# Kernel tuning notes

Measured on AMD Instinct MI355X. Metric: run time of the kernel, lower is better.

The kernel has to match this reference:

```python
import jax, jax.numpy as jnp
import numpy as np

D = 100  # hard-coded model dim from the source
L, BS = 4096, 64


def setup_inputs() -> dict:
    key = jax.random.key(0)
    k_x, k_w, k_b, k_s = jax.random.split(key, 4)
    x = jax.random.normal(k_x, (L, BS, 1, D), dtype=jnp.float32)
    # nn.Linear(D, D): weight [D, D] (out, in), bias [D]
    lim = 1.0 / np.sqrt(D)
    W = jax.random.uniform(k_w, (D, D), dtype=jnp.float32, minval=-lim, maxval=lim)
    b = jax.random.uniform(k_b, (D,), dtype=jnp.float32, minval=-lim, maxval=lim)
    # self.states ~ Normal(0, 0.02), shape [D, D]
    states = 0.02 * jax.random.normal(k_s, (D, D), dtype=jnp.float32)
    return {"x": x, "W": W, "b": b, "states": states}


def reference(x, W, b, states):
    # z1 = layer1(x): x [L, BS, 1, D] @ W.T + b
    z1 = jnp.einsum("lbod,ed->lboe", x, W) + b
    # scan: carry = tile(states) is constant across steps (f multiplies by 1.0),
    # so output[i] = z1[i] @ states for every timestep -> one fused batched matmul.
    out = jnp.einsum("lbod,de->lboe", z1, states)
    return out
```

## Files before the change

kernel.cpp:

```cpp
#include <hip/hip_runtime.h>

typedef __bf16 bf16x8 __attribute__((ext_vector_type(8)));
typedef float  f32x4  __attribute__((ext_vector_type(4)));

#define D100 100
#define NROWS (4096*64)
#define NTILES (NROWS/16)
#define NCT 7
#define NKS 4
#define FRAG_ELEMS (NCT*NKS*64*8)
#define NBLK (NTILES/8)

__global__ __launch_bounds__(256) void prep_kernel(
    const float* __restrict__ W, const float* __restrict__ bvec,
    const float* __restrict__ S, __bf16* __restrict__ wsM) {
  int tid = blockIdx.x * 256 + threadIdx.x;
  if (tid >= FRAG_ELEMS) return;
  int j    = tid & 7;
  int lane = (tid >> 3) & 63;
  int ks   = (tid >> 9) & 3;
  int ct   = tid >> 11;
  int k = ks * 32 + ((lane >> 4) * 8) + j;
  int n = ct * 16 + (lane & 15);
  float acc = 0.f;
  if (n < D100) {
    if (k < D100) {
      float a0 = 0.f, a1 = 0.f, a2 = 0.f, a3 = 0.f;
      for (int d = 0; d < D100; d += 4) {
        a0 += W[(d + 0) * D100 + k] * S[(d + 0) * D100 + n];
        a1 += W[(d + 1) * D100 + k] * S[(d + 1) * D100 + n];
        a2 += W[(d + 2) * D100 + k] * S[(d + 2) * D100 + n];
        a3 += W[(d + 3) * D100 + k] * S[(d + 3) * D100 + n];
      }
      acc = (a0 + a1) + (a2 + a3);
    } else if (k == 112) {
      for (int d = 0; d < D100; ++d) acc += bvec[d] * S[d * D100 + n];
    }
  }
  wsM[tid] = (__bf16)acc;
}

__global__ __launch_bounds__(512, 8) void gemm_kernel(
    const float* __restrict__ x, const __bf16* __restrict__ wsM,
    float* __restrict__ out) {
  __shared__ __align__(16) __bf16 ldsB[FRAG_ELEMS];

  const int t    = threadIdx.x;
  const int lane = t & 63;
  const int l16  = lane & 15;
  const int lg   = lane >> 4;
  const int tile = blockIdx.x * 8 + (t >> 6);

  const float* xr = x + (size_t)tile * (16 * D100) + l16 * D100;
  f32x4 xv[7];
#pragma unroll
  for (int ks = 0; ks < 3; ++ks) {
    xv[ks * 2]     = *(const f32x4*)(xr + ks * 32 + lg * 8);
    xv[ks * 2 + 1] = *(const f32x4*)(xr + ks * 32 + lg * 8 + 4);
  }
  xv[6] = (lg == 0) ? *(const f32x4*)(xr + 96) : (f32x4){0.f, 0.f, 0.f, 0.f};

  {
    const f32x4* src = (const f32x4*)wsM;
    f32x4*       dst = (f32x4*)ldsB;
    dst[t]        = src[t];
    dst[512 + t]  = src[512 + t];
    dst[1024 + t] = src[1024 + t];
    if (t < 256) dst[1536 + t] = src[1536 + t];
  }
  __syncthreads();

  f32x4 acc[NCT];
#pragma unroll
  for (int ct = 0; ct < NCT; ++ct) acc[ct] = (f32x4){0.f, 0.f, 0.f, 0.f};

  const bf16x8* Bv = (const bf16x8*)ldsB;
#pragma unroll
  for (int ks = 0; ks < NKS; ++ks) {
    bf16x8 xf;
    if (ks < 3) {
      f32x4 v0 = xv[ks * 2], v1 = xv[ks * 2 + 1];
#pragma unroll
      for (int j = 0; j < 4; ++j) {
        xf[j]     = (__bf16)v0[j];
        xf[j + 4] = (__bf16)v1[j];
      }
    } else {
      f32x4 v0 = xv[6];
#pragma unroll
      for (int j = 0; j < 4; ++j) {
        xf[j]     = (__bf16)v0[j];
        xf[j + 4] = (__bf16)0.f;
      }
      if (lg == 2) xf[0] = (__bf16)1.0f;
    }
#pragma unroll
    for (int ct = 0; ct < NCT; ++ct)
      acc[ct] = __builtin_amdgcn_mfma_f32_16x16x32_bf16(
          Bv[(ct * NKS + ks) * 64 + lane], xf, acc[ct], 0, 0, 0);
  }

  float* orow = out + (size_t)tile * (16 * D100) + l16 * D100 + lg * 4;
#pragma unroll
  for (int ct = 0; ct < NCT; ++ct) {
    if (ct < 6 || lg == 0)
      *(f32x4*)(orow + ct * 16) = acc[ct];
  }
}

extern "C" void kernel_launch(void* const* d_in, const int* in_sizes, int n_in,
                              void* d_out, int out_size, void* d_ws,
                              size_t ws_size, hipStream_t stream) {
  const float* x = (const float*)d_in[0];
  const float* W = (const float*)d_in[1];
  const float* b = (const float*)d_in[2];
  const float* S = (const float*)d_in[3];
  __bf16* wsM = (__bf16*)d_ws;
  float*  out = (float*)d_out;

  hipLaunchKernelGGL(prep_kernel, dim3(56), dim3(256), 0, stream,
                     W, b, S, wsM);
  hipLaunchKernelGGL(gemm_kernel, dim3(NBLK), dim3(512), 0, stream,
                     x, wsM, out);
}
```

Baseline: 49.85 us.

## Stage x tiles and output through LDS with direct global-to-LDS loads

Replaces the per-lane strided row loads of x with direct global_load_lds copies of each wave's contiguous 6400-byte tile into shared memory, then reads MFMA operands from LDS. The B fragments are loaded the same way. Results are written to LDS and then stored to global memory as fully contiguous 16-byte-per-lane chunks, so loads and stores are coalesced. This adds 51KB of LDS per block and lowers the occupancy hint from 8 to 4, which may reduce latency hiding.

```diff
diff --git a/kernel.cpp b/kernel.cpp
--- a/kernel.cpp
+++ b/kernel.cpp
@@ -9,7 +9,11 @@
 #define NCT 7
 #define NKS 4
 #define FRAG_ELEMS (NCT*NKS*64*8)
+#define TILE_B 6400
 #define NBLK (NTILES/8)
+
+typedef const __attribute__((address_space(1))) void gvoid;
+typedef __attribute__((address_space(3))) void lvoid;
 
 __global__ __launch_bounds__(256) void prep_kernel(
     const float* __restrict__ W, const float* __restrict__ bvec,
@@ -40,33 +44,35 @@
   wsM[tid] = (__bf16)acc;
 }
 
-__global__ __launch_bounds__(512, 8) void gemm_kernel(
+__global__ __launch_bounds__(512, 4) void gemm_kernel(
     const float* __restrict__ x, const __bf16* __restrict__ wsM,
     float* __restrict__ out) {
   __shared__ __align__(16) __bf16 ldsB[FRAG_ELEMS];
+  __shared__ __align__(16) float  ldsX[8 * 1600];
 
   const int t    = threadIdx.x;
   const int lane = t & 63;
   const int l16  = lane & 15;
   const int lg   = lane >> 4;
-  const int tile = blockIdx.x * 8 + (t >> 6);
+  const int w    = t >> 6;
+  const int tile = blockIdx.x * 8 + w;
 
-  const float* xr = x + (size_t)tile * (16 * D100) + l16 * D100;
-  f32x4 xv[7];
+  const char* xsrc = (const char*)x + (size_t)tile * TILE_B + (size_t)lane * 16;
+  char* ldsx = (char*)(ldsX + w * 1600);
 #pragma unroll
-  for (int ks = 0; ks < 3; ++ks) {
-    xv[ks * 2]     = *(const f32x4*)(xr + ks * 32 + lg * 8);
-    xv[ks * 2 + 1] = *(const f32x4*)(xr + ks * 32 + lg * 8 + 4);
-  }
-  xv[6] = (lg == 0) ? *(const f32x4*)(xr + 96) : (f32x4){0.f, 0.f, 0.f, 0.f};
+  for (int c = 0; c < 6; ++c)
+    __builtin_amdgcn_global_load_lds((gvoid*)(xsrc + c * 1024),
+                                     (lvoid*)(ldsx + c * 1024), 16, 0, 0);
+  if (lane < 16)
+    __builtin_amdgcn_global_load_lds((gvoid*)(xsrc + 6144),
+                                     (lvoid*)(ldsx + 6144), 16, 0, 0);
 
   {
-    const f32x4* src = (const f32x4*)wsM;
-    f32x4*       dst = (f32x4*)ldsB;
-    dst[t]        = src[t];
-    dst[512 + t]  = src[512 + t];
-    dst[1024 + t] = src[1024 + t];
-    if (t < 256) dst[1536 + t] = src[1536 + t];
+    const char* bsrc = (const char*)wsM + (size_t)lane * 16;
+    for (int c = w; c < 28; c += 8)
+      __builtin_amdgcn_global_load_lds((gvoid*)(bsrc + c * 1024),
+                                       (lvoid*)((char*)ldsB + c * 1024),
+                                       16, 0, 0);
   }
   __syncthreads();
 
@@ -75,18 +81,22 @@
   for (int ct = 0; ct < NCT; ++ct) acc[ct] = (f32x4){0.f, 0.f, 0.f, 0.f};
 
   const bf16x8* Bv = (const bf16x8*)ldsB;
+  const char* xrow = ldsx + l16 * 400;
+
 #pragma unroll
   for (int ks = 0; ks < NKS; ++ks) {
     bf16x8 xf;
     if (ks < 3) {
-      f32x4 v0 = xv[ks * 2], v1 = xv[ks * 2 + 1];
+      f32x4 v0 = *(const f32x4*)(xrow + ks * 128 + lg * 32);
+      f32x4 v1 = *(const f32x4*)(xrow + ks * 128 + lg * 32 + 16);
 #pragma unroll
       for (int j = 0; j < 4; ++j) {
         xf[j]     = (__bf16)v0[j];
         xf[j + 4] = (__bf16)v1[j];
       }
     } else {
-      f32x4 v0 = xv[6];
+      f32x4 v0 = (lg == 0) ? *(const f32x4*)(xrow + 384)
+                           : (f32x4){0.f, 0.f, 0.f, 0.f};
 #pragma unroll
       for (int j = 0; j < 4; ++j) {
         xf[j]     = (__bf16)v0[j];
@@ -100,11 +110,21 @@
           Bv[(ct * NKS + ks) * 64 + lane], xf, acc[ct], 0, 0, 0);
   }
 
-  float* orow = out + (size_t)tile * (16 * D100) + l16 * D100 + lg * 4;
 #pragma unroll
   for (int ct = 0; ct < NCT; ++ct) {
     if (ct < 6 || lg == 0)
-      *(f32x4*)(orow + ct * 16) = acc[ct];
+      *(f32x4*)(ldsx + l16 * 400 + ct * 64 + lg * 16) = acc[ct];
+  }
+
+  char* dst = (char*)(out + (size_t)tile * 1600) + (size_t)lane * 16;
+#pragma unroll
+  for (int c = 0; c < 6; ++c) {
+    f32x4 v = *(const f32x4*)(ldsx + c * 1024 + lane * 16);
+    *(f32x4*)(dst + c * 1024) = v;
+  }
+  if (lane < 16) {
+    f32x4 v = *(const f32x4*)(ldsx + 6144 + lane * 16);
+    *(f32x4*)(dst + 6144) = v;
   }
 }
 
```

New measurement: 45.18 us. 9.4% less time.
